# Kernel optimization log

Hardware: AMD Instinct MI355X
Metric: run time of the kernel (lower is better)

## Reference

```python
import jax, jax.numpy as jnp
import numpy as np

L = 8      # number of history layers backsubstituted (history[2:] in the torch code)
D = 2048   # layer width


def setup_inputs() -> dict:
    key = jax.random.key(0)
    ks = jax.random.split(key, 8)
    lower = jax.random.normal(ks[6], (D,), dtype=jnp.float32)
    upper = lower + jax.random.uniform(ks[7], (D,), dtype=jnp.float32)  # ensure lower <= upper
    return {
        "A": jax.random.normal(ks[0], (D, D), dtype=jnp.float32) * 0.05,
        "b": jax.random.normal(ks[1], (D,), dtype=jnp.float32) * 0.05,
        "hist_Al": jax.random.normal(ks[2], (L, D, D), dtype=jnp.float32) * 0.05,
        "hist_Au": jax.random.normal(ks[3], (L, D, D), dtype=jnp.float32) * 0.05,
        "hist_bl": jax.random.normal(ks[4], (L, D), dtype=jnp.float32) * 0.05,
        "hist_bu": jax.random.normal(ks[5], (L, D), dtype=jnp.float32) * 0.05,
        "lower_in": lower,
        "upper_in": upper,
    }


def reference(A, b, hist_Al, hist_Au, hist_bl, hist_bu, lower_in, upper_in):
    # Affine layer sets Al = Au = A, bl = bu = b, then backsubstitutes
    # through the history in reverse order (torch loop: i = len-1 .. 2).
    def step(carry, dp):
        Al, Au, bl, bu = carry
        dAl, dAu, dbl, dbu = dp
        Al_pos = jnp.maximum(Al, 0.0)
        Al_neg = jnp.minimum(Al, 0.0)
        Au_pos = jnp.maximum(Au, 0.0)
        Au_neg = jnp.minimum(Au, 0.0)
        new_Al = Al_pos @ dAl + Al_neg @ dAu
        new_bl = Al_pos @ dbl + Al_neg @ dbu + bl
        new_Au = Au_pos @ dAu + Au_neg @ dAl
        new_bu = Au_pos @ dbu + Au_neg @ dbl + bu
        return (new_Al, new_Au, new_bl, new_bu), None

    init = (A, A, b, b)
    # reverse the history so scan walks from the last layer back to the first
    dps = (hist_Al[::-1], hist_Au[::-1], hist_bl[::-1], hist_bu[::-1])
    (Al, Au, bl, bu), _ = jax.lax.scan(step, init, dps)

    # final concretization against the input box (history[1] in the torch code)
    lower = jnp.maximum(Al, 0.0) @ lower_in + jnp.minimum(Al, 0.0) @ upper_in + bl
    upper = jnp.maximum(Au, 0.0) @ upper_in + jnp.minimum(Au, 0.0) @ lower_in + bu
    return lower, upper
```

## Files before the change

kernel.cpp:

```cpp
#include <hip/hip_runtime.h>
#include <cstdint>
#include <cstddef>

#define D 2048
#define L 8
#define KS 2048
#define BM 256
#define BNR 256
#define BK 32
#define NT (KS / BK)
#define BUFSZ ((BM + BNR) * BK)

typedef _Float16 f16;
typedef _Float16 f16x4 __attribute__((ext_vector_type(4)));
typedef _Float16 f16x8 __attribute__((ext_vector_type(8)));
typedef float f32x4 __attribute__((ext_vector_type(4)));
typedef unsigned int u32x4 __attribute__((ext_vector_type(4)));

__device__ __forceinline__ void gload16(const void* g, void* l) {
  __builtin_amdgcn_global_load_lds(
      (const __attribute__((address_space(1))) void*)g,
      (__attribute__((address_space(3))) void*)l, 16, 0, 0);
}

__global__ __launch_bounds__(256) void k_init(
    const float* __restrict__ A, const float* __restrict__ b,
    const float* __restrict__ db1, const float* __restrict__ db2,
    f16* __restrict__ Ab, float* __restrict__ blbu, float* __restrict__ outacc) {
  const int m = blockIdx.x, tid = threadIdx.x;
  if (m < 2) {
    f32x4 z = {0.f, 0.f, 0.f, 0.f};
    *(f32x4*)(outacc + m * 2048 + tid * 8) = z;
    *(f32x4*)(outacc + m * 2048 + tid * 8 + 4) = z;
  }
  const int k = tid * 8;
  size_t i = (size_t)m * D + k;
  f32x4 a0 = *(const f32x4*)(A + i);
  f32x4 a1 = *(const f32x4*)(A + i + 4);
  f16x8 h;
  float cL = 0.f, cU = 0.f;
#pragma unroll
  for (int j = 0; j < 8; ++j) {
    float v = (j < 4) ? a0[j] : a1[j - 4];
    h[j] = (f16)v;
    float pf = fmaxf(v, 0.f), nf = fminf(v, 0.f);
    float w1 = db1[k + j], w2 = db2[k + j];
    cL += pf * w1 + nf * w2;
    cU += pf * w2 + nf * w1;
  }
  *(f16x8*)(Ab + (size_t)m * KS + k) = h;
  *(f16x8*)(Ab + (size_t)(D + m) * KS + k) = h;

  __shared__ float redL[4], redU[4];
#pragma unroll
  for (int off = 32; off > 0; off >>= 1) {
    cL += __shfl_down(cL, off);
    cU += __shfl_down(cU, off);
  }
  const int wave = tid >> 6, lane = tid & 63;
  if (lane == 0) { redL[wave] = cL; redU[wave] = cU; }
  __syncthreads();
  if (tid == 0) {
    float bL = b[m] + redL[0] + redL[1] + redL[2] + redL[3];
    float bU = b[m] + redU[0] + redU[1] + redU[2] + redU[3];
    blbu[m] = bL; blbu[D + m] = bU;
  }
}

__global__ __launch_bounds__(512) void k_prep(
    const float* __restrict__ srcAl, const float* __restrict__ srcAu,
    f16* __restrict__ Bb) {
  const int p = blockIdx.x, tid = threadIdx.x;
  const size_t MS = (size_t)D * D;
  const int col = (p & 31) * 64 + (tid & 63);
  const int k0 = (p >> 5) * 64 + (tid >> 6) * 8;
  float sl[8], su[8];
#pragma unroll
  for (int j = 0; j < 8; ++j) {
    sl[j] = srcAl[(size_t)(k0 + j) * D + col];
    su[j] = srcAu[(size_t)(k0 + j) * D + col];
  }
  f16x8 hs, hd;
#pragma unroll
  for (int j = 0; j < 8; ++j) {
    hs[j] = (f16)((sl[j] + su[j]) * 0.5f);
    hd[j] = (f16)((sl[j] - su[j]) * 0.5f);
  }
  *(f16x8*)(Bb + (size_t)col * KS + k0) = hs;
  *(f16x8*)(Bb + MS + (size_t)col * KS + k0) = hd;
}

__global__ __launch_bounds__(512, 2) void k_gemm(
    const f16* __restrict__ A,
    const f16* __restrict__ Bb,
    f16* __restrict__ BTn,
    const float* __restrict__ nAl, const float* __restrict__ nAu,
    const float* __restrict__ w1, const float* __restrict__ w2,
    float* __restrict__ bdst,
    f16* __restrict__ An,
    const int do_tr, const int wstate) {
  __shared__ __align__(16) f16 lds[4 * BUFSZ];
  const size_t MS = (size_t)D * D;

  const int flat = blockIdx.x;
  const int xcd = flat & 7, idx = flat >> 3;
  const int by = (xcd >> 1) * 4 + (idx >> 3);
  const int bx = (xcd & 1) * 8 + (idx & 7);
  const int m0 = by * BM;
  const int n0 = bx * 128;

  const int tid = threadIdx.x;
  const int wave = tid >> 6, lane = tid & 63;
  const int wm = (wave & 3) * 64, wn = (wave >> 2) * 64;
  const int lr = lane & 15, lq = lane >> 4;
  const int srow = lane >> 2;
  const int scol = ((lane & 3) ^ ((lane >> 3) & 3)) * 8;
  const int rchunk = (lq ^ ((lr >> 1) & 3)) * 8;
  const int low = (m0 < D) ? 1 : 0;
  const unsigned amask = low ? 0x7FFF7FFFu : 0xFFFFFFFFu;
  const unsigned omask = low ? 0x00000000u : 0x80008000u;

  const f16* Bs = Bb;
  const f16* Bd = Bb + MS;

  f32x4 acc[4][4];
#pragma unroll
  for (int m = 0; m < 4; ++m)
#pragma unroll
    for (int n = 0; n < 4; ++n)
      acc[m][n] = (f32x4){0.f, 0.f, 0.f, 0.f};

  auto stage = [&](int kt, int buf) {
    f16* bA = lds + buf * BUFSZ;
    f16* bB = bA + BM * BK;
    const size_t gk = (size_t)kt * BK;
    gload16(A + (size_t)(m0 + wave * 16 + srow) * KS + gk + scol,
            bA + wave * 512);
    gload16(A + (size_t)(m0 + (wave + 8) * 16 + srow) * KS + gk + scol,
            bA + (wave + 8) * 512);
    gload16(Bs + (size_t)(n0 + wave * 16 + srow) * KS + gk + scol,
            bB + wave * 512);
    gload16(Bd + (size_t)(n0 + wave * 16 + srow) * KS + gk + scol,
            bB + (wave + 8) * 512);
  };

  stage(0, 0); stage(1, 1); stage(2, 2);
  asm volatile("s_waitcnt vmcnt(8)" ::: "memory");
  __builtin_amdgcn_sched_barrier(0);
  __builtin_amdgcn_s_barrier();
  __builtin_amdgcn_sched_barrier(0);

  float trl[8], tru[8];

  for (int t = 0; t < NT; ++t) {
    const f16* bA = lds + (t & 3) * BUFSZ;
    const f16* bB = bA + BM * BK;
    const int tmod = t & 15;

    if (do_tr && tmod == 6) {
      const int p = flat * 4 + ((t - 6) >> 4);
      const int col = (p & 31) * 64 + (tid & 63);
      const int k0 = (p >> 5) * 64 + (tid >> 6) * 8;
      f16x8 hs, hd;
#pragma unroll
      for (int j = 0; j < 8; ++j) {
        hs[j] = (f16)((trl[j] + tru[j]) * 0.5f);
        hd[j] = (f16)((trl[j] - tru[j]) * 0.5f);
      }
      *(f16x8*)(BTn + (size_t)col * KS + k0) = hs;
      *(f16x8*)(BTn + MS + (size_t)col * KS + k0) = hd;
    }
    if (do_tr && tmod == 2) {
      const int p = flat * 4 + ((t - 2) >> 4);
      const int col = (p & 31) * 64 + (tid & 63);
      const int k0 = (p >> 5) * 64 + (tid >> 6) * 8;
#pragma unroll
      for (int j = 0; j < 8; ++j) {
        trl[j] = nAl[(size_t)(k0 + j) * D + col];
        tru[j] = nAu[(size_t)(k0 + j) * D + col];
      }
    }
    __builtin_amdgcn_sched_barrier(0);

    if (t + 3 < NT) stage(t + 3, (t + 3) & 3);

    f16x8 a[4], bs4[4], bd4[4], ax[4];
#pragma unroll
    for (int m = 0; m < 4; ++m)
      a[m] = *(const f16x8*)(bA + (wm + m * 16 + lr) * BK + rchunk);
#pragma unroll
    for (int n = 0; n < 4; ++n)
      bs4[n] = *(const f16x8*)(bB + (wn + n * 16 + lr) * BK + rchunk);
#pragma unroll
    for (int n = 0; n < 4; ++n)
      bd4[n] = *(const f16x8*)(bB + (128 + wn + n * 16 + lr) * BK + rchunk);
#pragma unroll
    for (int m = 0; m < 4; ++m) {
      u32x4 u = *(const u32x4*)&a[m];
      u = (u & amask) | omask;
      ax[m] = *(const f16x8*)&u;
    }
    __builtin_amdgcn_s_setprio(1);
#pragma unroll
    for (int m = 0; m < 4; ++m)
#pragma unroll
      for (int n = 0; n < 4; ++n)
        acc[m][n] = __builtin_amdgcn_mfma_f32_16x16x32_f16(
            bs4[n], a[m], acc[m][n], 0, 0, 0);
#pragma unroll
    for (int m = 0; m < 4; ++m)
#pragma unroll
      for (int n = 0; n < 4; ++n)
        acc[m][n] = __builtin_amdgcn_mfma_f32_16x16x32_f16(
            bd4[n], ax[m], acc[m][n], 0, 0, 0);
    __builtin_amdgcn_s_setprio(0);

    if (t + 3 < NT) {
      if (do_tr && (tmod == 2 || tmod == 3)) {
        asm volatile("s_waitcnt vmcnt(24)" ::: "memory");
      } else {
        asm volatile("s_waitcnt vmcnt(8)" ::: "memory");
      }
    } else if (t + 1 < NT) {
      asm volatile("s_waitcnt vmcnt(0)" ::: "memory");
    }
    __builtin_amdgcn_sched_barrier(0);
    __builtin_amdgcn_s_barrier();
    __builtin_amdgcn_sched_barrier(0);
  }

  f32x4 w1v[4], w2v[4];
#pragma unroll
  for (int n = 0; n < 4; ++n) {
    const int col = n0 + wn + n * 16 + lq * 4;
    w1v[n] = *(const f32x4*)(w1 + col);
    w2v[n] = *(const f32x4*)(w2 + col);
  }
  float rowsum[4] = {0.f, 0.f, 0.f, 0.f};
#pragma unroll
  for (int m = 0; m < 4; ++m) {
#pragma unroll
    for (int n = 0; n < 4; ++n) {
      const size_t row = (size_t)(m0 + wm + m * 16 + lr);
      const int col = n0 + wn + n * 16 + lq * 4;
      f16x4 h;
#pragma unroll
      for (int r = 0; r < 4; ++r) {
        float v = acc[m][n][r];
        float pf = fmaxf(v, 0.f), qf = fminf(v, 0.f);
        h[r] = (f16)v;
        float wa = low ? w1v[n][r] : w2v[n][r];
        float wb = low ? w2v[n][r] : w1v[n][r];
        rowsum[m] += pf * wa + qf * wb;
      }
      if (wstate)
        *(f16x4*)(An + row * KS + col) = h;
    }
  }
#pragma unroll
  for (int m = 0; m < 4; ++m) {
    float v = rowsum[m];
    v += __shfl_down(v, 32);
    v += __shfl_down(v, 16);
    if (lane < 16)
      atomicAdd(bdst + m0 + wm + m * 16 + lane, v);
  }
}

__global__ __launch_bounds__(256) void k_final(
    const float* __restrict__ outacc, const float* __restrict__ blbu,
    float* __restrict__ out) {
  const int R = blockIdx.x * 256 + threadIdx.x;
  out[R] = outacc[R] + blbu[R];
}

extern "C" void kernel_launch(void* const* d_in, const int* in_sizes, int n_in,
                              void* d_out, int out_size, void* d_ws, size_t ws_size,
                              hipStream_t stream) {
  (void)in_sizes; (void)n_in; (void)out_size;
  const float* A   = (const float*)d_in[0];
  const float* b   = (const float*)d_in[1];
  const float* hAl = (const float*)d_in[2];
  const float* hAu = (const float*)d_in[3];
  const float* hbl = (const float*)d_in[4];
  const float* hbu = (const float*)d_in[5];
  const float* lo  = (const float*)d_in[6];
  const float* up  = (const float*)d_in[7];
  float* out = (float*)d_out;

  const size_t AS = (size_t)2 * D * KS;
  const size_t BS = (size_t)2 * D * D;
  const size_t MS = (size_t)D * D;
  char* base = (char*)d_ws;
  f16* Ab0   = (f16*)base;
  f16* Ab1   = Ab0 + AS;
  f16* Bb0   = Ab1 + AS;
  float* blbu   = (float*)(Bb0 + BS);
  float* outacc = blbu + 2 * D;
  f16* Bb1   = (f16*)(outacc + 2 * D);
  const size_t need_fused = (size_t)((char*)(Bb1 + BS) - base);
  const bool fused = ws_size >= need_fused;

  k_init<<<dim3(D), 256, 0, stream>>>(
      A, b, hbl + (size_t)7 * D, hbu + (size_t)7 * D, Ab0, blbu, outacc);
  k_prep<<<dim3(1024), 512, 0, stream>>>(
      hAl + (size_t)7 * MS, hAu + (size_t)7 * MS, Bb0);

  f16* cur = Ab0;
  f16* nxt = Ab1;
  for (int t = 0; t < L; ++t) {
    const int nlayer = 6 - t;
    const float* w1 = (t < 7) ? hbl + (size_t)nlayer * D : lo;
    const float* w2 = (t < 7) ? hbu + (size_t)nlayer * D : up;
    float* bd = (t < 7) ? blbu : outacc;
    f16* BT  = (fused && (t & 1)) ? Bb1 : Bb0;
    f16* BTn = fused ? ((t & 1) ? Bb0 : Bb1) : Bb0;
    const float* nl = (t < 7) ? hAl + (size_t)nlayer * MS : hAl;
    const float* nu = (t < 7) ? hAu + (size_t)nlayer * MS : hAu;
    if (!fused && t > 0)
      k_prep<<<dim3(1024), 512, 0, stream>>>(
          hAl + (size_t)(7 - t) * MS, hAu + (size_t)(7 - t) * MS, Bb0);
    const int do_tr = (fused && t < 7) ? 1 : 0;
    const int wstate = (t < 7) ? 1 : 0;
    k_gemm<<<dim3(256), 512, 0, stream>>>(cur, BT, BTn, nl, nu, w1, w2, bd,
                                          nxt, do_tr, wstate);
    f16* tmp = cur; cur = nxt; nxt = tmp;
  }
  k_final<<<dim3(2 * D / 256), 256, 0, stream>>>(outacc, blbu, out);
}
```

Before: 670.5 us.

## Halve GEMM M-tile to 128 with 4-wave blocks and 3-stage LDS pipeline

Shrinks the k_gemm block tile from 256x128 to 128x128, uses 256-thread blocks with four waves, and launches 512 blocks instead of 256. The LDS ring drops from four stages to three, with prefetch depth and vmcnt waits adjusted to match. The fused transpose-prep work is re-split so each thread handles 16 rows instead of 8. The aim is more blocks per CU and better load balance, at the cost of less B-tile reuse per block, a shallower prefetch pipeline, and more register pressure from the larger transpose buffers.

```diff
diff --git a/kernel.cpp b/kernel.cpp
--- a/kernel.cpp
+++ b/kernel.cpp
@@ -5,11 +5,11 @@
 #define D 2048
 #define L 8
 #define KS 2048
-#define BM 256
-#define BNR 256
+#define BM 128
+#define BN 128
 #define BK 32
 #define NT (KS / BK)
-#define BUFSZ ((BM + BNR) * BK)
+#define BUFSZ ((BM + 2 * BN) * BK)
 
 typedef _Float16 f16;
 typedef _Float16 f16x4 __attribute__((ext_vector_type(4)));
@@ -90,7 +90,7 @@
   *(f16x8*)(Bb + MS + (size_t)col * KS + k0) = hd;
 }
 
-__global__ __launch_bounds__(512, 2) void k_gemm(
+__global__ __launch_bounds__(256, 2) void k_gemm(
     const f16* __restrict__ A,
     const f16* __restrict__ Bb,
     f16* __restrict__ BTn,
@@ -99,19 +99,19 @@
     float* __restrict__ bdst,
     f16* __restrict__ An,
     const int do_tr, const int wstate) {
-  __shared__ __align__(16) f16 lds[4 * BUFSZ];
+  __shared__ __align__(16) f16 lds[3 * BUFSZ];
   const size_t MS = (size_t)D * D;
 
   const int flat = blockIdx.x;
   const int xcd = flat & 7, idx = flat >> 3;
-  const int by = (xcd >> 1) * 4 + (idx >> 3);
+  const int by = (xcd >> 1) * 8 + (idx >> 3);
   const int bx = (xcd & 1) * 8 + (idx & 7);
   const int m0 = by * BM;
-  const int n0 = bx * 128;
+  const int n0 = bx * BN;
 
   const int tid = threadIdx.x;
   const int wave = tid >> 6, lane = tid & 63;
-  const int wm = (wave & 3) * 64, wn = (wave >> 2) * 64;
+  const int wm = (wave >> 1) * 64, wn = (wave & 1) * 64;
   const int lr = lane & 15, lq = lane >> 4;
   const int srow = lane >> 2;
   const int scol = ((lane & 3) ^ ((lane >> 3) & 3)) * 8;
@@ -134,55 +134,66 @@
     f16* bA = lds + buf * BUFSZ;
     f16* bB = bA + BM * BK;
     const size_t gk = (size_t)kt * BK;
-    gload16(A + (size_t)(m0 + wave * 16 + srow) * KS + gk + scol,
-            bA + wave * 512);
-    gload16(A + (size_t)(m0 + (wave + 8) * 16 + srow) * KS + gk + scol,
-            bA + (wave + 8) * 512);
-    gload16(Bs + (size_t)(n0 + wave * 16 + srow) * KS + gk + scol,
-            bB + wave * 512);
-    gload16(Bd + (size_t)(n0 + wave * 16 + srow) * KS + gk + scol,
-            bB + (wave + 8) * 512);
+#pragma unroll
+    for (int i = 0; i < 2; ++i) {
+      const int c = i * 4 + wave;
+      gload16(A + (size_t)(m0 + c * 16 + srow) * KS + gk + scol, bA + c * 512);
+    }
+#pragma unroll
+    for (int i = 0; i < 2; ++i) {
+      const int c = i * 4 + wave;
+      gload16(Bs + (size_t)(n0 + c * 16 + srow) * KS + gk + scol, bB + c * 512);
+    }
+#pragma unroll
+    for (int i = 0; i < 2; ++i) {
+      const int c = i * 4 + wave;
+      gload16(Bd + (size_t)(n0 + c * 16 + srow) * KS + gk + scol,
+              bB + (8 + c) * 512);
+    }
   };
 
-  stage(0, 0); stage(1, 1); stage(2, 2);
-  asm volatile("s_waitcnt vmcnt(8)" ::: "memory");
+  stage(0, 0); stage(1, 1);
+  asm volatile("s_waitcnt vmcnt(6)" ::: "memory");
   __builtin_amdgcn_sched_barrier(0);
   __builtin_amdgcn_s_barrier();
   __builtin_amdgcn_sched_barrier(0);
 
-  float trl[8], tru[8];
+  float trl[16], tru[16];
 
   for (int t = 0; t < NT; ++t) {
-    const f16* bA = lds + (t & 3) * BUFSZ;
+    const f16* bA = lds + (t % 3) * BUFSZ;
     const f16* bB = bA + BM * BK;
-    const int tmod = t & 15;
+    const int tmod = t & 31;
 
     if (do_tr && tmod == 6) {
-      const int p = flat * 4 + ((t - 6) >> 4);
+      const int p = flat * 2 + (t >> 5);
       const int col = (p & 31) * 64 + (tid & 63);
-      const int k0 = (p >> 5) * 64 + (tid >> 6) * 8;
-      f16x8 hs, hd;
+      const int k0 = (p >> 5) * 64 + (tid >> 6) * 16;
+      f16x8 hs0, hd0, hs1, hd1;
 #pragma unroll
       for (int j = 0; j < 8; ++j) {
-        hs[j] = (f16)((trl[j] + tru[j]) * 0.5f);
-        hd[j] = (f16)((trl[j] - tru[j]) * 0.5f);
+        hs0[j] = (f16)((trl[j] + tru[j]) * 0.5f);
+        hd0[j] = (f16)((trl[j] - tru[j]) * 0.5f);
+        hs1[j] = (f16)((trl[8 + j] + tru[8 + j]) * 0.5f);
+        hd1[j] = (f16)((trl[8 + j] - tru[8 + j]) * 0.5f);
       }
-      *(f16x8*)(BTn + (size_t)col * KS + k0) = hs;
-      *(f16x8*)(BTn + MS + (size_t)col * KS + k0) = hd;
+      f16* ds = BTn + (size_t)col * KS + k0;
+      *(f16x8*)ds = hs0;            *(f16x8*)(ds + 8) = hs1;
+      *(f16x8*)(ds + MS) = hd0;     *(f16x8*)(ds + MS + 8) = hd1;
     }
     if (do_tr && tmod == 2) {
-      const int p = flat * 4 + ((t - 2) >> 4);
+      const int p = flat * 2 + (t >> 5);
       const int col = (p & 31) * 64 + (tid & 63);
-      const int k0 = (p >> 5) * 64 + (tid >> 6) * 8;
-#pragma unroll
-      for (int j = 0; j < 8; ++j) {
+      const int k0 = (p >> 5) * 64 + (tid >> 6) * 16;
+#pragma unroll
+      for (int j = 0; j < 16; ++j) {
         trl[j] = nAl[(size_t)(k0 + j) * D + col];
         tru[j] = nAu[(size_t)(k0 + j) * D + col];
       }
     }
     __builtin_amdgcn_sched_barrier(0);
 
-    if (t + 3 < NT) stage(t + 3, (t + 3) & 3);
+    if (t + 2 < NT) stage(t + 2, (t + 2) % 3);
 
     f16x8 a[4], bs4[4], bd4[4], ax[4];
 #pragma unroll
@@ -215,11 +226,11 @@
             bd4[n], ax[m], acc[m][n], 0, 0, 0);
     __builtin_amdgcn_s_setprio(0);
 
-    if (t + 3 < NT) {
-      if (do_tr && (tmod == 2 || tmod == 3)) {
-        asm volatile("s_waitcnt vmcnt(24)" ::: "memory");
+    if (t + 2 < NT) {
+      if (do_tr && tmod == 2) {
+        asm volatile("s_waitcnt vmcnt(38)" ::: "memory");
       } else {
-        asm volatile("s_waitcnt vmcnt(8)" ::: "memory");
+        asm volatile("s_waitcnt vmcnt(6)" ::: "memory");
       }
     } else if (t + 1 < NT) {
       asm volatile("s_waitcnt vmcnt(0)" ::: "memory");
@@ -322,7 +333,7 @@
           hAl + (size_t)(7 - t) * MS, hAu + (size_t)(7 - t) * MS, Bb0);
     const int do_tr = (fused && t < 7) ? 1 : 0;
     const int wstate = (t < 7) ? 1 : 0;
-    k_gemm<<<dim3(256), 512, 0, stream>>>(cur, BT, BTn, nl, nu, w1, w2, bd,
+    k_gemm<<<dim3(512), 256, 0, stream>>>(cur, BT, BTn, nl, nu, w1, w2, bd,
                                           nxt, do_tr, wstate);
     f16* tmp = cur; cur = nxt; nxt = tmp;
   }
```

Measured after the change: 703.6 us. 1.05x slower.

## Load A operand directly to registers and double BK with 3-stage LDS pipeline

Applied to the files above, without the earlier changes.

The A tile is no longer staged through LDS. Each wave loads its A fragments straight from global memory into registers, ping-ponging them one step ahead, while only the B tiles (sum and diff halves) go through LDS. BK doubles to 64 with a 3-buffer ring and an 8-way XOR swizzle, which halves the number of barriers per K sweep and removes A's LDS writes and reads. The cost is more VGPR pressure from holding two A register sets, and the A global reads are redundant across the two column-waves that share rows.

```diff
diff --git a/kernel.cpp b/kernel.cpp
--- a/kernel.cpp
+++ b/kernel.cpp
@@ -6,10 +6,11 @@
 #define L 8
 #define KS 2048
 #define BM 256
-#define BNR 256
-#define BK 32
+#define BN 128
+#define BK 64
 #define NT (KS / BK)
-#define BUFSZ ((BM + BNR) * BK)
+#define BROWS 256
+#define BUFSZ (BROWS * BK)
 
 typedef _Float16 f16;
 typedef _Float16 f16x4 __attribute__((ext_vector_type(4)));
@@ -99,7 +100,7 @@
     float* __restrict__ bdst,
     f16* __restrict__ An,
     const int do_tr, const int wstate) {
-  __shared__ __align__(16) f16 lds[4 * BUFSZ];
+  __shared__ __align__(16) f16 lds[3 * BUFSZ];
   const size_t MS = (size_t)D * D;
 
   const int flat = blockIdx.x;
@@ -107,19 +108,17 @@
   const int by = (xcd >> 1) * 4 + (idx >> 3);
   const int bx = (xcd & 1) * 8 + (idx & 7);
   const int m0 = by * BM;
-  const int n0 = bx * 128;
+  const int n0 = bx * BN;
 
   const int tid = threadIdx.x;
   const int wave = tid >> 6, lane = tid & 63;
   const int wm = (wave & 3) * 64, wn = (wave >> 2) * 64;
   const int lr = lane & 15, lq = lane >> 4;
-  const int srow = lane >> 2;
-  const int scol = ((lane & 3) ^ ((lane >> 3) & 3)) * 8;
-  const int rchunk = (lq ^ ((lr >> 1) & 3)) * 8;
+  const int sub = lane >> 3;
+  const int cg = ((lane & 7) ^ sub) * 8;
   const int low = (m0 < D) ? 1 : 0;
   const unsigned amask = low ? 0x7FFF7FFFu : 0xFFFFFFFFu;
   const unsigned omask = low ? 0x00000000u : 0x80008000u;
-
   const f16* Bs = Bb;
   const f16* Bd = Bb + MS;
 
@@ -130,103 +129,115 @@
     for (int n = 0; n < 4; ++n)
       acc[m][n] = (f32x4){0.f, 0.f, 0.f, 0.f};
 
-  auto stage = [&](int kt, int buf) {
-    f16* bA = lds + buf * BUFSZ;
-    f16* bB = bA + BM * BK;
+  auto stageB = [&](int kt, int buf) {
+    f16* bB = lds + buf * BUFSZ;
     const size_t gk = (size_t)kt * BK;
-    gload16(A + (size_t)(m0 + wave * 16 + srow) * KS + gk + scol,
-            bA + wave * 512);
-    gload16(A + (size_t)(m0 + (wave + 8) * 16 + srow) * KS + gk + scol,
-            bA + (wave + 8) * 512);
-    gload16(Bs + (size_t)(n0 + wave * 16 + srow) * KS + gk + scol,
-            bB + wave * 512);
-    gload16(Bd + (size_t)(n0 + wave * 16 + srow) * KS + gk + scol,
-            bB + (wave + 8) * 512);
+#pragma unroll
+    for (int i = 0; i < 4; ++i) {
+      const int r = i * 8 + wave;
+      const int row = r * 8 + sub;
+      const f16* src = (r < 16) ? (Bs + (size_t)(n0 + row) * KS)
+                                : (Bd + (size_t)(n0 + row - 128) * KS);
+      gload16(src + gk + cg, bB + r * 512);
+    }
   };
 
-  stage(0, 0); stage(1, 1); stage(2, 2);
-  asm volatile("s_waitcnt vmcnt(8)" ::: "memory");
+  auto loadA = [&](int kt, f16x8 (&a)[2][4]) {
+    const size_t gk = (size_t)kt * BK;
+#pragma unroll
+    for (int kb = 0; kb < 2; ++kb)
+#pragma unroll
+      for (int m = 0; m < 4; ++m)
+        a[kb][m] = *(const f16x8*)(A + (size_t)(m0 + wm + m * 16 + lr) * KS
+                                   + gk + kb * 32 + lq * 8);
+  };
+
+  auto compute = [&](const f16* bB, f16x8 (&a)[2][4]) {
+#pragma unroll
+    for (int kb = 0; kb < 2; ++kb) {
+      f16x8 bs4[4], bd4[4];
+#pragma unroll
+      for (int n = 0; n < 4; ++n) {
+        const int row = wn + n * 16 + lr;
+        const int ch = ((kb * 4 + lq) ^ (lr & 7)) * 8;
+        bs4[n] = *(const f16x8*)(bB + row * BK + ch);
+        bd4[n] = *(const f16x8*)(bB + (128 + row) * BK + ch);
+      }
+      __builtin_amdgcn_s_setprio(1);
+#pragma unroll
+      for (int m = 0; m < 4; ++m) {
+        u32x4 u = *(const u32x4*)&a[kb][m];
+        u = (u & amask) | omask;
+        f16x8 axm = *(const f16x8*)&u;
+#pragma unroll
+        for (int n = 0; n < 4; ++n) {
+          acc[m][n] = __builtin_amdgcn_mfma_f32_16x16x32_f16(
+              bs4[n], a[kb][m], acc[m][n], 0, 0, 0);
+          acc[m][n] = __builtin_amdgcn_mfma_f32_16x16x32_f16(
+              bd4[n], axm, acc[m][n], 0, 0, 0);
+        }
+      }
+      __builtin_amdgcn_s_setprio(0);
+    }
+  };
+
+  float trl[8], tru[8];
+
+  auto body = [&](int t, f16x8 (&aCur)[2][4], f16x8 (&aNxt)[2][4]) {
+    const f16* bB = lds + (t % 3) * BUFSZ;
+    const int tmod = t & 7;
+    if (do_tr && tmod == 6) {
+      const int p = flat * 4 + (t >> 3);
+      const int col = (p & 31) * 64 + (tid & 63);
+      const int k0 = (p >> 5) * 64 + (tid >> 6) * 8;
+      f16x8 hs, hd;
+#pragma unroll
+      for (int j = 0; j < 8; ++j) {
+        hs[j] = (f16)((trl[j] + tru[j]) * 0.5f);
+        hd[j] = (f16)((trl[j] - tru[j]) * 0.5f);
+      }
+      *(f16x8*)(BTn + (size_t)col * KS + k0) = hs;
+      *(f16x8*)(BTn + MS + (size_t)col * KS + k0) = hd;
+    }
+    if (do_tr && tmod == 2) {
+      const int p = flat * 4 + (t >> 3);
+      const int col = (p & 31) * 64 + (tid & 63);
+      const int k0 = (p >> 5) * 64 + (tid >> 6) * 8;
+#pragma unroll
+      for (int j = 0; j < 8; ++j) {
+        trl[j] = nAl[(size_t)(k0 + j) * D + col];
+        tru[j] = nAu[(size_t)(k0 + j) * D + col];
+      }
+    }
+    __builtin_amdgcn_sched_barrier(0);
+    if (t + 1 < NT) loadA(t + 1, aNxt);
+    if (t + 2 < NT) stageB(t + 2, (t + 2) % 3);
+    compute(bB, aCur);
+    if (t + 2 < NT) {
+      if (do_tr && tmod == 2)
+        asm volatile("s_waitcnt vmcnt(28)" ::: "memory");
+      else
+        asm volatile("s_waitcnt vmcnt(12)" ::: "memory");
+    } else if (t + 1 < NT) {
+      asm volatile("s_waitcnt vmcnt(8)" ::: "memory");
+    }
+    __builtin_amdgcn_sched_barrier(0);
+    __builtin_amdgcn_s_barrier();
+    __builtin_amdgcn_sched_barrier(0);
+  };
+
+  f16x8 aA[2][4], aB[2][4];
+  loadA(0, aA);
+  stageB(0, 0);
+  stageB(1, 1);
+  asm volatile("s_waitcnt vmcnt(4)" ::: "memory");
   __builtin_amdgcn_sched_barrier(0);
   __builtin_amdgcn_s_barrier();
   __builtin_amdgcn_sched_barrier(0);
 
-  float trl[8], tru[8];
-
-  for (int t = 0; t < NT; ++t) {
-    const f16* bA = lds + (t & 3) * BUFSZ;
-    const f16* bB = bA + BM * BK;
-    const int tmod = t & 15;
-
-    if (do_tr && tmod == 6) {
-      const int p = flat * 4 + ((t - 6) >> 4);
-      const int col = (p & 31) * 64 + (tid & 63);
-      const int k0 = (p >> 5) * 64 + (tid >> 6) * 8;
-      f16x8 hs, hd;
-#pragma unroll
-      for (int j = 0; j < 8; ++j) {
-        hs[j] = (f16)((trl[j] + tru[j]) * 0.5f);
-        hd[j] = (f16)((trl[j] - tru[j]) * 0.5f);
-      }
-      *(f16x8*)(BTn + (size_t)col * KS + k0) = hs;
-      *(f16x8*)(BTn + MS + (size_t)col * KS + k0) = hd;
-    }
-    if (do_tr && tmod == 2) {
-      const int p = flat * 4 + ((t - 2) >> 4);
-      const int col = (p & 31) * 64 + (tid & 63);
-      const int k0 = (p >> 5) * 64 + (tid >> 6) * 8;
-#pragma unroll
-      for (int j = 0; j < 8; ++j) {
-        trl[j] = nAl[(size_t)(k0 + j) * D + col];
-        tru[j] = nAu[(size_t)(k0 + j) * D + col];
-      }
-    }
-    __builtin_amdgcn_sched_barrier(0);
-
-    if (t + 3 < NT) stage(t + 3, (t + 3) & 3);
-
-    f16x8 a[4], bs4[4], bd4[4], ax[4];
-#pragma unroll
-    for (int m = 0; m < 4; ++m)
-      a[m] = *(const f16x8*)(bA + (wm + m * 16 + lr) * BK + rchunk);
-#pragma unroll
-    for (int n = 0; n < 4; ++n)
-      bs4[n] = *(const f16x8*)(bB + (wn + n * 16 + lr) * BK + rchunk);
-#pragma unroll
-    for (int n = 0; n < 4; ++n)
-      bd4[n] = *(const f16x8*)(bB + (128 + wn + n * 16 + lr) * BK + rchunk);
-#pragma unroll
-    for (int m = 0; m < 4; ++m) {
-      u32x4 u = *(const u32x4*)&a[m];
-      u = (u & amask) | omask;
-      ax[m] = *(const f16x8*)&u;
-    }
-    __builtin_amdgcn_s_setprio(1);
-#pragma unroll
-    for (int m = 0; m < 4; ++m)
-#pragma unroll
-      for (int n = 0; n < 4; ++n)
-        acc[m][n] = __builtin_amdgcn_mfma_f32_16x16x32_f16(
-            bs4[n], a[m], acc[m][n], 0, 0, 0);
-#pragma unroll
-    for (int m = 0; m < 4; ++m)
-#pragma unroll
-      for (int n = 0; n < 4; ++n)
-        acc[m][n] = __builtin_amdgcn_mfma_f32_16x16x32_f16(
-            bd4[n], ax[m], acc[m][n], 0, 0, 0);
-    __builtin_amdgcn_s_setprio(0);
-
-    if (t + 3 < NT) {
-      if (do_tr && (tmod == 2 || tmod == 3)) {
-        asm volatile("s_waitcnt vmcnt(24)" ::: "memory");
-      } else {
-        asm volatile("s_waitcnt vmcnt(8)" ::: "memory");
-      }
-    } else if (t + 1 < NT) {
-      asm volatile("s_waitcnt vmcnt(0)" ::: "memory");
-    }
-    __builtin_amdgcn_sched_barrier(0);
-    __builtin_amdgcn_s_barrier();
-    __builtin_amdgcn_sched_barrier(0);
+  for (int tt = 0; tt < NT; tt += 2) {
+    body(tt, aA, aB);
+    body(tt + 1, aB, aA);
   }
 
   f32x4 w1v[4], w2v[4];
```

Result: slower. 874.0 us (+30.4%).

## Double K tile to 64 and switch GEMM to double-buffered LDS pipeline

Applied to the files above, without the earlier changes.

Raises the K tile from 32 to 64 and replaces the 4-stage, 3-ahead LDS prefetch ring with a 2-buffer, 1-ahead scheme. Each iteration now runs two MFMA sub-steps, with a new XOR swizzle over 8 chunks to avoid LDS bank conflicts. The transposition side work is rescheduled to the new iteration count. The kernel waits on vmcnt(0) every iteration and occupancy drops to one block per CU, so less load latency is hidden in exchange for half as many barriers.

```diff
diff --git a/kernel.cpp b/kernel.cpp
--- a/kernel.cpp
+++ b/kernel.cpp
@@ -6,10 +6,12 @@
 #define L 8
 #define KS 2048
 #define BM 256
-#define BNR 256
-#define BK 32
+#define BN 128
+#define BK 64
 #define NT (KS / BK)
-#define BUFSZ ((BM + BNR) * BK)
+#define AROWS 256
+#define BROWS 256
+#define BUFSZ ((AROWS + BROWS) * BK)
 
 typedef _Float16 f16;
 typedef _Float16 f16x4 __attribute__((ext_vector_type(4)));
@@ -90,7 +92,7 @@
   *(f16x8*)(Bb + MS + (size_t)col * KS + k0) = hd;
 }
 
-__global__ __launch_bounds__(512, 2) void k_gemm(
+__global__ __launch_bounds__(512, 1) void k_gemm(
     const f16* __restrict__ A,
     const f16* __restrict__ Bb,
     f16* __restrict__ BTn,
@@ -99,7 +101,7 @@
     float* __restrict__ bdst,
     f16* __restrict__ An,
     const int do_tr, const int wstate) {
-  __shared__ __align__(16) f16 lds[4 * BUFSZ];
+  __shared__ __align__(16) f16 lds[2 * BUFSZ];
   const size_t MS = (size_t)D * D;
 
   const int flat = blockIdx.x;
@@ -107,19 +109,17 @@
   const int by = (xcd >> 1) * 4 + (idx >> 3);
   const int bx = (xcd & 1) * 8 + (idx & 7);
   const int m0 = by * BM;
-  const int n0 = bx * 128;
+  const int n0 = bx * BN;
 
   const int tid = threadIdx.x;
   const int wave = tid >> 6, lane = tid & 63;
   const int wm = (wave & 3) * 64, wn = (wave >> 2) * 64;
   const int lr = lane & 15, lq = lane >> 4;
-  const int srow = lane >> 2;
-  const int scol = ((lane & 3) ^ ((lane >> 3) & 3)) * 8;
-  const int rchunk = (lq ^ ((lr >> 1) & 3)) * 8;
+  const int sub = lane >> 3;
+  const int cg = ((lane & 7) ^ sub) * 8;
   const int low = (m0 < D) ? 1 : 0;
   const unsigned amask = low ? 0x7FFF7FFFu : 0xFFFFFFFFu;
   const unsigned omask = low ? 0x00000000u : 0x80008000u;
-
   const f16* Bs = Bb;
   const f16* Bd = Bb + MS;
 
@@ -132,20 +132,28 @@
 
   auto stage = [&](int kt, int buf) {
     f16* bA = lds + buf * BUFSZ;
-    f16* bB = bA + BM * BK;
+    f16* bB = bA + AROWS * BK;
     const size_t gk = (size_t)kt * BK;
-    gload16(A + (size_t)(m0 + wave * 16 + srow) * KS + gk + scol,
-            bA + wave * 512);
-    gload16(A + (size_t)(m0 + (wave + 8) * 16 + srow) * KS + gk + scol,
-            bA + (wave + 8) * 512);
-    gload16(Bs + (size_t)(n0 + wave * 16 + srow) * KS + gk + scol,
-            bB + wave * 512);
-    gload16(Bd + (size_t)(n0 + wave * 16 + srow) * KS + gk + scol,
-            bB + (wave + 8) * 512);
+#pragma unroll
+    for (int i = 0; i < 4; ++i) {
+      const int r = i * 8 + wave;
+      gload16(A + (size_t)(m0 + r * 8 + sub) * KS + gk + cg, bA + r * 512);
+    }
+#pragma unroll
+    for (int i = 0; i < 2; ++i) {
+      const int r = i * 8 + wave;
+      gload16(Bs + (size_t)(n0 + r * 8 + sub) * KS + gk + cg, bB + r * 512);
+    }
+#pragma unroll
+    for (int i = 0; i < 2; ++i) {
+      const int r = i * 8 + wave;
+      gload16(Bd + (size_t)(n0 + r * 8 + sub) * KS + gk + cg,
+              bB + (16 + r) * 512);
+    }
   };
 
-  stage(0, 0); stage(1, 1); stage(2, 2);
-  asm volatile("s_waitcnt vmcnt(8)" ::: "memory");
+  stage(0, 0);
+  asm volatile("s_waitcnt vmcnt(0)" ::: "memory");
   __builtin_amdgcn_sched_barrier(0);
   __builtin_amdgcn_s_barrier();
   __builtin_amdgcn_sched_barrier(0);
@@ -153,12 +161,12 @@
   float trl[8], tru[8];
 
   for (int t = 0; t < NT; ++t) {
-    const f16* bA = lds + (t & 3) * BUFSZ;
-    const f16* bB = bA + BM * BK;
-    const int tmod = t & 15;
-
-    if (do_tr && tmod == 6) {
-      const int p = flat * 4 + ((t - 6) >> 4);
+    const f16* bA = lds + (t & 1) * BUFSZ;
+    const f16* bB = bA + AROWS * BK;
+    const int tmod = t & 7;
+
+    if (do_tr && tmod == 4) {
+      const int p = flat * 4 + (t >> 3);
       const int col = (p & 31) * 64 + (tid & 63);
       const int k0 = (p >> 5) * 64 + (tid >> 6) * 8;
       f16x8 hs, hd;
@@ -171,7 +179,7 @@
       *(f16x8*)(BTn + MS + (size_t)col * KS + k0) = hd;
     }
     if (do_tr && tmod == 2) {
-      const int p = flat * 4 + ((t - 2) >> 4);
+      const int p = flat * 4 + (t >> 3);
       const int col = (p & 31) * 64 + (tid & 63);
       const int k0 = (p >> 5) * 64 + (tid >> 6) * 8;
 #pragma unroll
@@ -182,48 +190,45 @@
     }
     __builtin_amdgcn_sched_barrier(0);
 
-    if (t + 3 < NT) stage(t + 3, (t + 3) & 3);
-
-    f16x8 a[4], bs4[4], bd4[4], ax[4];
-#pragma unroll
-    for (int m = 0; m < 4; ++m)
-      a[m] = *(const f16x8*)(bA + (wm + m * 16 + lr) * BK + rchunk);
-#pragma unroll
-    for (int n = 0; n < 4; ++n)
-      bs4[n] = *(const f16x8*)(bB + (wn + n * 16 + lr) * BK + rchunk);
-#pragma unroll
-    for (int n = 0; n < 4; ++n)
-      bd4[n] = *(const f16x8*)(bB + (128 + wn + n * 16 + lr) * BK + rchunk);
-#pragma unroll
-    for (int m = 0; m < 4; ++m) {
-      u32x4 u = *(const u32x4*)&a[m];
-      u = (u & amask) | omask;
-      ax[m] = *(const f16x8*)&u;
-    }
-    __builtin_amdgcn_s_setprio(1);
-#pragma unroll
-    for (int m = 0; m < 4; ++m)
-#pragma unroll
-      for (int n = 0; n < 4; ++n)
-        acc[m][n] = __builtin_amdgcn_mfma_f32_16x16x32_f16(
-            bs4[n], a[m], acc[m][n], 0, 0, 0);
-#pragma unroll
-    for (int m = 0; m < 4; ++m)
-#pragma unroll
-      for (int n = 0; n < 4; ++n)
-        acc[m][n] = __builtin_amdgcn_mfma_f32_16x16x32_f16(
-            bd4[n], ax[m], acc[m][n], 0, 0, 0);
-    __builtin_amdgcn_s_setprio(0);
-
-    if (t + 3 < NT) {
-      if (do_tr && (tmod == 2 || tmod == 3)) {
-        asm volatile("s_waitcnt vmcnt(24)" ::: "memory");
-      } else {
-        asm volatile("s_waitcnt vmcnt(8)" ::: "memory");
-      }
-    } else if (t + 1 < NT) {
-      asm volatile("s_waitcnt vmcnt(0)" ::: "memory");
-    }
+    if (t + 1 < NT) stage(t + 1, (t + 1) & 1);
+
+#pragma unroll
+    for (int ks = 0; ks < 2; ++ks) {
+      f16x8 a[4], bs4[4], bd4[4];
+#pragma unroll
+      for (int m = 0; m < 4; ++m)
+        a[m] = *(const f16x8*)(bA + (wm + m * 16 + lr) * BK
+                               + ((ks * 4 + lq) ^ (lane & 7)) * 8);
+#pragma unroll
+      for (int n = 0; n < 4; ++n) {
+        const int ch = ((ks * 4 + lq) ^ (lane & 7)) * 8;
+        bs4[n] = *(const f16x8*)(bB + (wn + n * 16 + lr) * BK + ch);
+        bd4[n] = *(const f16x8*)(bB + (128 + wn + n * 16 + lr) * BK + ch);
+      }
+      __builtin_amdgcn_s_setprio(1);
+#pragma unroll
+      for (int m = 0; m < 4; ++m)
+#pragma unroll
+        for (int n = 0; n < 4; ++n)
+          acc[m][n] = __builtin_amdgcn_mfma_f32_16x16x32_f16(
+              bs4[n], a[m], acc[m][n], 0, 0, 0);
+      f16x8 ax[4];
+#pragma unroll
+      for (int m = 0; m < 4; ++m) {
+        u32x4 u = *(const u32x4*)&a[m];
+        u = (u & amask) | omask;
+        ax[m] = *(const f16x8*)&u;
+      }
+#pragma unroll
+      for (int m = 0; m < 4; ++m)
+#pragma unroll
+        for (int n = 0; n < 4; ++n)
+          acc[m][n] = __builtin_amdgcn_mfma_f32_16x16x32_f16(
+              bd4[n], ax[m], acc[m][n], 0, 0, 0);
+      __builtin_amdgcn_s_setprio(0);
+    }
+
+    asm volatile("s_waitcnt vmcnt(0)" ::: "memory");
     __builtin_amdgcn_sched_barrier(0);
     __builtin_amdgcn_s_barrier();
     __builtin_amdgcn_sched_barrier(0);
```

Result: faster. 615.3 us (median of 2 runs) (-8.2%).
